# Performance work log

Measured on AMD Instinct MI355X. Metric: run time of the kernel, lower is better.

Reference implementation:

```python
import jax, jax.numpy as jnp
import numpy as np

N_CELLS = 2048
D_IN = 512
D_HID = 1024
D_OUT = 512
SYNC = 0.15
DEBATE = 0.15
N_FACTIONS = 8


def setup_inputs() -> dict:
    key = jax.random.key(0)
    ks = jax.random.split(key, 24)
    def w(k, shape, s=0.02):
        return jax.random.normal(k, shape, dtype=jnp.float32) * s
    ein = D_IN + D_HID          # complex-engine input dim (1536)
    gin = D_OUT + 1 + D_HID     # GRU gate input dim (1537)
    return {
        "x": jax.random.normal(ks[0], (1, D_IN), dtype=jnp.float32),
        "h_re": w(ks[1], (N_CELLS, D_HID), 0.1),
        "h_im": w(ks[2], (N_CELLS, D_HID), 0.1),
        "ea_wr": w(ks[3], (ein, D_OUT)), "ea_br": w(ks[4], (D_OUT,)),
        "ea_wi": w(ks[5], (ein, D_OUT)), "ea_bi": w(ks[6], (D_OUT,)),
        "eg_wr": w(ks[7], (ein, D_OUT)), "eg_br": w(ks[8], (D_OUT,)),
        "eg_wi": w(ks[9], (ein, D_OUT)), "eg_bi": w(ks[10], (D_OUT,)),
        "gz_w": w(ks[11], (gin, D_HID)), "gz_b": w(ks[12], (D_HID,)),
        "gr_w": w(ks[13], (gin, D_HID)), "gr_b": w(ks[14], (D_HID,)),
        "ghr_w": w(ks[15], (gin, D_HID)), "ghr_b": w(ks[16], (D_HID,)),
        "ghi_w": w(ks[17], (gin, D_HID)), "ghi_b": w(ks[18], (D_HID,)),
        "oh_w": w(ks[19], (2 * D_OUT, D_IN)), "oh_b": w(ks[20], (D_IN,)),
        "step": 7,
    }


def _clin(a, b, Wr, br, Wi, bi):
    # complex linear: (Wr + iWi)(a + ib) with torch's bias semantics
    return (a @ Wr + br) - (b @ Wi + bi), (b @ Wr + br) + (a @ Wi + bi)


def reference(x, h_re, h_im, ea_wr, ea_br, ea_wi, ea_bi, eg_wr, eg_br, eg_wi, eg_bi,
              gz_w, gz_b, gr_w, gr_b, ghr_w, ghr_b, ghi_w, ghi_b, oh_w, oh_b, step):
    # batch the 256-cell Python loop into single GEMMs over the cell axis
    xb = jnp.broadcast_to(x, (N_CELLS, D_IN))
    c_re = jnp.concatenate([xb, h_re], -1)                       # [N, D_IN+D_HID]
    c_im = jnp.concatenate([jnp.zeros_like(xb), h_im], -1)
    a_re, a_im = _clin(c_re, c_im, ea_wr, ea_br, ea_wi, ea_bi)
    g_re, g_im = _clin(c_re, c_im, eg_wr, eg_br, eg_wi, eg_bi)
    o_re, o_im = a_re - g_re, a_im - g_im                        # [N, D_OUT]
    tension = jnp.mean(o_re**2 + o_im**2, -1)                    # [N]

    # GRU memory update (detached input, matching output.detach())
    so_re = jax.lax.stop_gradient(o_re)
    so_im = jax.lax.stop_gradient(o_im)
    t_sg = jax.lax.stop_gradient(tension)
    mem_re = jnp.concatenate([so_re, t_sg[:, None]], -1)         # [N, D_OUT+1]
    mem_im = jnp.concatenate([so_im, jnp.zeros((N_CELLS, 1), o_im.dtype)], -1)
    x_mag = jnp.sqrt(mem_re**2 + mem_im**2)
    h_mag = jnp.sqrt(h_re**2 + h_im**2)
    cm = jnp.concatenate([x_mag, h_mag], -1)                     # [N, D_OUT+1+D_HID]
    z = jax.nn.sigmoid(cm @ gz_w + gz_b)
    r = jax.nn.sigmoid(cm @ gr_w + gr_b)
    comb_r = jnp.concatenate([mem_re, r * h_re], -1)
    comb_i = jnp.concatenate([mem_im, r * h_im], -1)
    cand_re = jnp.tanh(comb_r @ ghr_w + ghr_b)
    cand_im = jnp.tanh(comb_i @ ghi_w + ghi_b)
    nh_re = jax.lax.stop_gradient((1 - z) * h_re + z * cand_re)
    nh_im = jax.lax.stop_gradient((1 - z) * h_im + z * cand_im)

    # faction sync + debate (linear op, applied per component)
    fs = N_CELLS // N_FACTIONS
    def sync(h):
        hf = h.reshape(N_FACTIONS, fs, D_HID)
        hf = (1 - SYNC) * hf + SYNC * jnp.mean(hf, 1, keepdims=True)
        if step > 5:
            glob = jnp.mean(jnp.mean(hf, 1), 0)                  # [D_HID]
            dc = max(1, fs // 4)
            hf = hf.at[:, :dc].set((1 - DEBATE) * hf[:, :dc] + DEBATE * glob)
        return hf.reshape(N_CELLS, D_HID)
    nh_re, nh_im = sync(nh_re), sync(nh_im)

    # tension-softmax-weighted combination (weights are non-differentiable, .item() in torch)
    w_soft = jax.nn.softmax(t_sg)                                # [N]
    comb_re = (w_soft[:, None] * o_re).sum(0, keepdims=True)     # [1, D_OUT]
    comb_im = (w_soft[:, None] * o_im).sum(0, keepdims=True)
    out_real = jnp.concatenate([comb_re, comb_im], -1)           # [1, 2*D_OUT]
    pred = out_real @ oh_w + oh_b                                # [1, D_IN]
    return pred, jnp.mean(tension), nh_re, nh_im
```

## Files before the change

### kernel.cpp

```cpp
#include <hip/hip_runtime.h>
#include <math.h>

#define N_CELLS 2048
#define D_IN 512
#define D_HID 1024
#define D_OUT 512

typedef __attribute__((ext_vector_type(8))) short bf16x8;
typedef __attribute__((ext_vector_type(4))) float f32x4;
typedef __attribute__((ext_vector_type(4))) short short4v;

#define MFMA16(a, b, c) __builtin_amdgcn_mfma_f32_16x16x32_bf16(a, b, c, 0, 0, 0)

__device__ __forceinline__ short f2bf(float f) {
  union { float f; unsigned u; } v; v.f = f;
  unsigned r = (v.u + 0x7FFFu + ((v.u >> 16) & 1u)) >> 16;
  return (short)r;
}

__device__ __forceinline__ void gl_lds16(const void* g, void* l) {
  __builtin_amdgcn_global_load_lds(
      (const __attribute__((address_space(1))) void*)g,
      (__attribute__((address_space(3))) void*)l, 16, 0, 0);
}

__global__ __launch_bounds__(256) void k_transpose_all(
    const float* __restrict__ w0, const float* __restrict__ w1,
    const float* __restrict__ w2, const float* __restrict__ w3,
    short* __restrict__ t0, short* __restrict__ t1,
    short* __restrict__ t2, short* __restrict__ t3,
    const float* __restrict__ ea_wr, const float* __restrict__ eg_wr,
    const float* __restrict__ ea_wi, const float* __restrict__ eg_wi,
    short* __restrict__ wdrT, short* __restrict__ wdiT, short* __restrict__ wdnT) {
  const int k0 = blockIdx.x * 32, n0 = blockIdx.y * 32;
  const int c = threadIdx.x & 31, r4 = threadIdx.x >> 5;
  if (blockIdx.z < 4) {
    const float* w = (blockIdx.z == 0) ? w0 : (blockIdx.z == 1) ? w1
                   : (blockIdx.z == 2) ? w2 : w3;
    short* wT = (blockIdx.z == 0) ? t0 : (blockIdx.z == 1) ? t1
              : (blockIdx.z == 2) ? t2 : t3;
    __shared__ float t[32][33];
#pragma unroll
    for (int i = 0; i < 4; ++i) {
      int kl = r4 * 4 + i;
      int k = k0 + kl;
      int srcrow = (k < 512) ? k : k + 1;
      t[kl][c] = w[(size_t)srcrow * D_HID + n0 + c];
    }
    __syncthreads();
#pragma unroll
    for (int i = 0; i < 4; ++i) {
      int nl = r4 * 4 + i;
      wT[(size_t)(n0 + nl) * 1536 + k0 + c] = f2bf(t[c][nl]);
    }
  } else {
    if (blockIdx.x >= 32 || blockIdx.y >= 16) return;
    __shared__ float tr[32][33], ti[32][33];
#pragma unroll
    for (int i = 0; i < 4; ++i) {
      int kl = r4 * 4 + i;
      int src = (512 + k0 + kl) * D_OUT + n0 + c;
      tr[kl][c] = ea_wr[src] - eg_wr[src];
      ti[kl][c] = ea_wi[src] - eg_wi[src];
    }
    __syncthreads();
#pragma unroll
    for (int i = 0; i < 4; ++i) {
      int nl = r4 * 4 + i;
      int dst = (n0 + nl) * D_HID + k0 + c;
      float dr = tr[c][nl], di = ti[c][nl];
      wdrT[dst] = f2bf(dr);
      wdiT[dst] = f2bf(di);
      wdnT[dst] = f2bf(-di);
    }
  }
}

__global__ __launch_bounds__(256) void k_prep_h(
    const float* __restrict__ h_re, const float* __restrict__ h_im,
    short* __restrict__ hbre, short* __restrict__ hbim, short* __restrict__ gatesA,
    float* __restrict__ tens) {
  if (threadIdx.x == 0) tens[blockIdx.x] = 0.f;
  int idx4 = (blockIdx.x * 256 + threadIdx.x) * 4;
  int m = idx4 >> 10, n = idx4 & 1023;
  float4 hr = *(const float4*)&h_re[idx4];
  float4 hi = *(const float4*)&h_im[idx4];
  short4v br, bi, bm;
  br.x = f2bf(hr.x); br.y = f2bf(hr.y); br.z = f2bf(hr.z); br.w = f2bf(hr.w);
  bi.x = f2bf(hi.x); bi.y = f2bf(hi.y); bi.z = f2bf(hi.z); bi.w = f2bf(hi.w);
  bm.x = f2bf(sqrtf(hr.x * hr.x + hi.x * hi.x));
  bm.y = f2bf(sqrtf(hr.y * hr.y + hi.y * hi.y));
  bm.z = f2bf(sqrtf(hr.z * hr.z + hi.z * hi.z));
  bm.w = f2bf(sqrtf(hr.w * hr.w + hi.w * hi.w));
  *(short4v*)&hbre[idx4] = br;
  *(short4v*)&hbim[idx4] = bi;
  *(short4v*)&gatesA[(size_t)m * 1536 + 512 + n] = bm;
}

__global__ __launch_bounds__(256) void k_bias_part(
    const float* __restrict__ x,
    const float* __restrict__ ea_wr, const float* __restrict__ ea_wi,
    const float* __restrict__ eg_wr, const float* __restrict__ eg_wi,
    float* __restrict__ bpartr, float* __restrict__ bparti) {
  int n = blockIdx.x * 256 + threadIdx.x;
  int kc = blockIdx.y;
  float sr = 0.f, si = 0.f;
  for (int i = 0; i < 64; ++i) {
    int k = kc * 64 + i;
    float xv = x[k];
    int idx = k * D_OUT + n;
    sr += xv * (ea_wr[idx] - eg_wr[idx]);
    si += xv * (ea_wi[idx] - eg_wi[idx]);
  }
  bpartr[kc * D_OUT + n] = sr;
  bparti[kc * D_OUT + n] = si;
}

__global__ __launch_bounds__(256) void k_bias_red(
    const float* __restrict__ bpartr, const float* __restrict__ bparti,
    const float* __restrict__ ea_br, const float* __restrict__ ea_bi,
    const float* __restrict__ eg_br, const float* __restrict__ eg_bi,
    float* __restrict__ bias_re, float* __restrict__ bias_im) {
  int n = blockIdx.x * 256 + threadIdx.x;
  float sr = 0.f, si = 0.f;
#pragma unroll
  for (int kc = 0; kc < 8; ++kc) { sr += bpartr[kc * D_OUT + n]; si += bparti[kc * D_OUT + n]; }
  float brd = ea_br[n] - eg_br[n];
  float bid = ea_bi[n] - eg_bi[n];
  bias_re[n] = sr + brd - bid;
  bias_im[n] = si + brd + bid;
}

__global__ __launch_bounds__(256) void k_engine(
    const short* __restrict__ hbre, const short* __restrict__ hbim,
    const short* __restrict__ wdrT, const short* __restrict__ wdiT,
    const short* __restrict__ wdnT,
    const float* __restrict__ bias_re, const float* __restrict__ bias_im,
    float* __restrict__ ore, float* __restrict__ oim,
    short* __restrict__ gatesA, short* __restrict__ candAre, short* __restrict__ candAim,
    float* __restrict__ tens) {
  __shared__ short Ar[2 * 64 * 32], Ai[2 * 64 * 32];
  __shared__ short Brs[2 * 32 * 32], Bis[2 * 32 * 32], Bns[2 * 32 * 32];
  const int m0 = blockIdx.x * 64, n0 = blockIdx.y * 32;
  const int tid = threadIdx.x;
  const int wid = tid >> 6, lane = tid & 63;
  const int quad = lane >> 4, lcol = lane & 15;
  const int wm = wid * 16;
  f32x4 accre[2], accim[2];
#pragma unroll
  for (int nt = 0; nt < 2; ++nt) {
    accre[nt] = (f32x4){0.f, 0.f, 0.f, 0.f};
    accim[nt] = (f32x4){0.f, 0.f, 0.f, 0.f};
  }
  for (int k0 = 0; k0 < D_HID; k0 += 64) {
    if (k0) __syncthreads();
#pragma unroll
    for (int i = 0; i < 2; ++i) {
      int c = i * 256 + tid;
      int kh = c >> 8, row = (c >> 2) & 63, kq = c & 3;
      size_t g = (size_t)(m0 + row) * D_HID + k0 + kh * 32 + kq * 8;
      gl_lds16(hbre + g, &Ar[c * 8]);
      gl_lds16(hbim + g, &Ai[c * 8]);
    }
    {
      int c = tid;
      int kh = c >> 7, row = (c >> 2) & 31, kq = c & 3;
      size_t g = (size_t)(n0 + row) * D_HID + k0 + kh * 32 + kq * 8;
      gl_lds16(wdrT + g, &Brs[c * 8]);
      gl_lds16(wdiT + g, &Bis[c * 8]);
      gl_lds16(wdnT + g, &Bns[c * 8]);
    }
    __syncthreads();
#pragma unroll
    for (int kh = 0; kh < 2; ++kh) {
      bf16x8 ar, ai, br[2], bi[2], bn[2];
      int aoff = kh * 2048 + (wm + lcol) * 32 + quad * 8;
      ar = *(const bf16x8*)&Ar[aoff];
      ai = *(const bf16x8*)&Ai[aoff];
#pragma unroll
      for (int nt = 0; nt < 2; ++nt) {
        int boff = kh * 1024 + (nt * 16 + lcol) * 32 + quad * 8;
        br[nt] = *(const bf16x8*)&Brs[boff];
        bi[nt] = *(const bf16x8*)&Bis[boff];
        bn[nt] = *(const bf16x8*)&Bns[boff];
      }
#pragma unroll
      for (int nt = 0; nt < 2; ++nt) {
        accre[nt] = MFMA16(ar, br[nt], accre[nt]);
        accre[nt] = MFMA16(ai, bn[nt], accre[nt]);
        accim[nt] = MFMA16(ar, bi[nt], accim[nt]);
        accim[nt] = MFMA16(ai, br[nt], accim[nt]);
      }
    }
  }
#pragma unroll
  for (int r = 0; r < 4; ++r) {
    int m = m0 + wm + quad * 4 + r;
    float t = 0.f;
#pragma unroll
    for (int nt = 0; nt < 2; ++nt) {
      int n = n0 + nt * 16 + lcol;
      float cre = accre[nt][r] + bias_re[n];
      float cim = accim[nt][r] + bias_im[n];
      t += cre * cre + cim * cim;
      ore[(size_t)m * D_OUT + n] = cre;
      oim[(size_t)m * D_OUT + n] = cim;
      gatesA[(size_t)m * 1536 + n] = f2bf(sqrtf(cre * cre + cim * cim));
      candAre[(size_t)m * 1536 + n] = f2bf(cre);
      candAim[(size_t)m * 1536 + n] = f2bf(cim);
    }
#pragma unroll
    for (int off = 1; off < 16; off <<= 1) t += __shfl_xor(t, off);
    if (lcol == 0) atomicAdd(&tens[m], t * (1.f / 512.f));
  }
}

__global__ __launch_bounds__(256) void k_gates(
    const short* __restrict__ gatesA,
    const short* __restrict__ gzwT, const short* __restrict__ grwT,
    const float* __restrict__ gz_w, const float* __restrict__ gz_b,
    const float* __restrict__ gr_w, const float* __restrict__ gr_b,
    const float* __restrict__ tens,
    const float* __restrict__ h_re, const float* __restrict__ h_im,
    float* __restrict__ zbuf,
    short* __restrict__ candAre, short* __restrict__ candAim) {
  __shared__ short As[2 * 128 * 32];
  __shared__ short Bs[2 * 64 * 32];
  const int is_z = (blockIdx.z == 0);
  const short* Bt = is_z ? gzwT : grwT;
  const int m0 = blockIdx.x * 128, n0 = blockIdx.y * 64;
  const int tid = threadIdx.x;
  const int wid = tid >> 6, lane = tid & 63;
  const int quad = lane >> 4, lcol = lane & 15;
  const int wm = (wid >> 1) * 64, wn = (wid & 1) * 32;
  f32x4 acc[4][2];
#pragma unroll
  for (int mt = 0; mt < 4; ++mt)
#pragma unroll
    for (int nt = 0; nt < 2; ++nt) acc[mt][nt] = (f32x4){0.f, 0.f, 0.f, 0.f};
  for (int k0 = 0; k0 < 1536; k0 += 64) {
    if (k0) __syncthreads();
#pragma unroll
    for (int i = 0; i < 4; ++i) {
      int c = i * 256 + tid;
      int kh = c >> 9, row = (c >> 2) & 127, kq = c & 3;
      gl_lds16(gatesA + (size_t)(m0 + row) * 1536 + k0 + kh * 32 + kq * 8, &As[c * 8]);
    }
#pragma unroll
    for (int i = 0; i < 2; ++i) {
      int c = i * 256 + tid;
      int kh = c >> 8, row = (c >> 2) & 63, kq = c & 3;
      gl_lds16(Bt + (size_t)(n0 + row) * 1536 + k0 + kh * 32 + kq * 8, &Bs[c * 8]);
    }
    __syncthreads();
#pragma unroll
    for (int kh = 0; kh < 2; ++kh) {
      bf16x8 a[4], b[2];
#pragma unroll
      for (int mt = 0; mt < 4; ++mt)
        a[mt] = *(const bf16x8*)&As[kh * 4096 + (wm + mt * 16 + lcol) * 32 + quad * 8];
#pragma unroll
      for (int nt = 0; nt < 2; ++nt)
        b[nt] = *(const bf16x8*)&Bs[kh * 2048 + (wn + nt * 16 + lcol) * 32 + quad * 8];
#pragma unroll
      for (int mt = 0; mt < 4; ++mt)
#pragma unroll
        for (int nt = 0; nt < 2; ++nt)
          acc[mt][nt] = MFMA16(a[mt], b[nt], acc[mt][nt]);
    }
  }
#pragma unroll
  for (int mt = 0; mt < 4; ++mt)
#pragma unroll
    for (int nt = 0; nt < 2; ++nt)
#pragma unroll
      for (int r = 0; r < 4; ++r) {
        int m = m0 + wm + mt * 16 + quad * 4 + r;
        int n = n0 + wn + nt * 16 + lcol;
        float tv = tens[m];
        if (is_z) {
          float zp = acc[mt][nt][r] + gz_b[n] + tv * gz_w[(size_t)512 * D_HID + n];
          zbuf[(size_t)m * D_HID + n] = 1.f / (1.f + expf(-zp));
        } else {
          float rp = acc[mt][nt][r] + gr_b[n] + tv * gr_w[(size_t)512 * D_HID + n];
          float rr = 1.f / (1.f + expf(-rp));
          candAre[(size_t)m * 1536 + 512 + n] = f2bf(rr * h_re[(size_t)m * D_HID + n]);
          candAim[(size_t)m * 1536 + 512 + n] = f2bf(rr * h_im[(size_t)m * D_HID + n]);
        }
      }
}

__global__ __launch_bounds__(256) void k_cand(
    const short* __restrict__ candAre, const short* __restrict__ candAim,
    const short* __restrict__ ghrwT, const short* __restrict__ ghiwT,
    const float* __restrict__ ghr_b, const float* __restrict__ ghi_b,
    const float* __restrict__ ghr_w,
    const float* __restrict__ tens, const float* __restrict__ zbuf,
    const float* __restrict__ h_re, const float* __restrict__ h_im,
    float* __restrict__ nhre, float* __restrict__ nhim) {
  __shared__ short As[2 * 128 * 32];
  __shared__ short Bs[2 * 64 * 32];
  const int is_re = (blockIdx.z == 0);
  const short* A = is_re ? candAre : candAim;
  const short* Bt = is_re ? ghrwT : ghiwT;
  const float* bias = is_re ? ghr_b : ghi_b;
  const float* h = is_re ? h_re : h_im;
  float* outp = is_re ? nhre : nhim;
  const int m0 = blockIdx.x * 128, n0 = blockIdx.y * 64;
  const int tid = threadIdx.x;
  const int wid = tid >> 6, lane = tid & 63;
  const int quad = lane >> 4, lcol = lane & 15;
  const int wm = (wid >> 1) * 64, wn = (wid & 1) * 32;
  f32x4 acc[4][2];
#pragma unroll
  for (int mt = 0; mt < 4; ++mt)
#pragma unroll
    for (int nt = 0; nt < 2; ++nt) acc[mt][nt] = (f32x4){0.f, 0.f, 0.f, 0.f};
  for (int k0 = 0; k0 < 1536; k0 += 64) {
    if (k0) __syncthreads();
#pragma unroll
    for (int i = 0; i < 4; ++i) {
      int c = i * 256 + tid;
      int kh = c >> 9, row = (c >> 2) & 127, kq = c & 3;
      gl_lds16(A + (size_t)(m0 + row) * 1536 + k0 + kh * 32 + kq * 8, &As[c * 8]);
    }
#pragma unroll
    for (int i = 0; i < 2; ++i) {
      int c = i * 256 + tid;
      int kh = c >> 8, row = (c >> 2) & 63, kq = c & 3;
      gl_lds16(Bt + (size_t)(n0 + row) * 1536 + k0 + kh * 32 + kq * 8, &Bs[c * 8]);
    }
    __syncthreads();
#pragma unroll
    for (int kh = 0; kh < 2; ++kh) {
      bf16x8 a[4], b[2];
#pragma unroll
      for (int mt = 0; mt < 4; ++mt)
        a[mt] = *(const bf16x8*)&As[kh * 4096 + (wm + mt * 16 + lcol) * 32 + quad * 8];
#pragma unroll
      for (int nt = 0; nt < 2; ++nt)
        b[nt] = *(const bf16x8*)&Bs[kh * 2048 + (wn + nt * 16 + lcol) * 32 + quad * 8];
#pragma unroll
      for (int mt = 0; mt < 4; ++mt)
#pragma unroll
        for (int nt = 0; nt < 2; ++nt)
          acc[mt][nt] = MFMA16(a[mt], b[nt], acc[mt][nt]);
    }
  }
#pragma unroll
  for (int mt = 0; mt < 4; ++mt)
#pragma unroll
    for (int nt = 0; nt < 2; ++nt)
#pragma unroll
      for (int r = 0; r < 4; ++r) {
        int m = m0 + wm + mt * 16 + quad * 4 + r;
        int n = n0 + wn + nt * 16 + lcol;
        float pre = acc[mt][nt][r] + bias[n];
        if (is_re) pre += tens[m] * ghr_w[(size_t)512 * D_HID + n];
        float cand = tanhf(pre);
        float z = zbuf[(size_t)m * D_HID + n];
        float hv = h[(size_t)m * D_HID + n];
        outp[(size_t)m * D_HID + n] = (1.f - z) * hv + z * cand;
      }
}

__global__ __launch_bounds__(256) void k_fsum_part(
    const float* __restrict__ nhre, const float* __restrict__ nhim,
    float* __restrict__ fpart) {
  int f = blockIdx.x >> 3, rc = blockIdx.x & 7, comp = blockIdx.y;
  const float* src = comp ? nhim : nhre;
  int row0 = f * 256 + rc * 32;
#pragma unroll
  for (int nc = 0; nc < 4; ++nc) {
    int n = nc * 256 + threadIdx.x;
    float s = 0.f;
    const float* base = src + (size_t)row0 * D_HID + n;
    for (int j = 0; j < 32; ++j) s += base[(size_t)j * D_HID];
    fpart[((size_t)comp * 64 + blockIdx.x) * D_HID + n] = s;
  }
}

__global__ __launch_bounds__(256) void k_fsum_red(
    const float* __restrict__ fpart,
    float* __restrict__ fsre, float* __restrict__ fsim,
    float* __restrict__ gre, float* __restrict__ gim) {
  int n = blockIdx.x * 256 + threadIdx.x;
  int comp = blockIdx.y;
  float* fs = comp ? fsim : fsre;
  float* g = comp ? gim : gre;
  float gsum = 0.f;
#pragma unroll
  for (int f = 0; f < 8; ++f) {
    float sf = 0.f;
#pragma unroll
    for (int rc = 0; rc < 8; ++rc)
      sf += fpart[((size_t)comp * 64 + f * 8 + rc) * D_HID + n];
    fs[f * D_HID + n] = sf;
    gsum += sf;
  }
  g[n] = gsum * (1.f / 2048.f);
}

__global__ __launch_bounds__(256) void k_sync(
    float* __restrict__ nhre, float* __restrict__ nhim,
    const float* __restrict__ fsre, const float* __restrict__ fsim,
    const float* __restrict__ gre, const float* __restrict__ gim,
    const int* __restrict__ step) {
  int idx = blockIdx.x * 256 + threadIdx.x;
  int m = idx >> 10, n = idx & 1023;
  int f = m >> 8;
  float vr = nhre[idx], vi = nhim[idx];
  vr = 0.85f * vr + 0.15f * (fsre[f * D_HID + n] * (1.f / 256.f));
  vi = 0.85f * vi + 0.15f * (fsim[f * D_HID + n] * (1.f / 256.f));
  if (step[0] > 5 && (m & 255) < 64) {
    vr = 0.85f * vr + 0.15f * gre[n];
    vi = 0.85f * vi + 0.15f * gim[n];
  }
  nhre[idx] = vr;
  nhim[idx] = vi;
}

__global__ __launch_bounds__(1024) void k_stats(
    const float* __restrict__ tens, float* __restrict__ wsoft,
    float* __restrict__ meanT_out) {
  __shared__ float red[16];
  __shared__ float s_max, s_sum;
  int tid = threadIdx.x;
  int wid = tid >> 6, lane = tid & 63;
  float a = tens[tid], b = tens[tid + 1024];
  float mx = fmaxf(a, b);
  for (int off = 32; off; off >>= 1) mx = fmaxf(mx, __shfl_down(mx, off));
  if (lane == 0) red[wid] = mx;
  __syncthreads();
  if (tid == 0) {
    float m2 = red[0];
    for (int i = 1; i < 16; ++i) m2 = fmaxf(m2, red[i]);
    s_max = m2;
  }
  __syncthreads();
  float mxv = s_max;
  float ea = expf(a - mxv), eb = expf(b - mxv);
  float se = ea + eb;
  for (int off = 32; off; off >>= 1) se += __shfl_down(se, off);
  __syncthreads();
  if (lane == 0) red[wid] = se;
  __syncthreads();
  if (tid == 0) {
    float s2 = 0.f;
    for (int i = 0; i < 16; ++i) s2 += red[i];
    s_sum = s2;
  }
  __syncthreads();
  float inv = 1.f / s_sum;
  wsoft[tid] = ea * inv;
  wsoft[tid + 1024] = eb * inv;
  float st = a + b;
  for (int off = 32; off; off >>= 1) st += __shfl_down(st, off);
  __syncthreads();
  if (lane == 0) red[wid] = st;
  __syncthreads();
  if (tid == 0) {
    float s2 = 0.f;
    for (int i = 0; i < 16; ++i) s2 += red[i];
    meanT_out[0] = s2 * (1.f / 2048.f);
  }
}

__global__ __launch_bounds__(256) void k_comb_part(
    const float* __restrict__ ore, const float* __restrict__ oim,
    const float* __restrict__ wsoft, float* __restrict__ cpart) {
  int j = blockIdx.x * 256 + threadIdx.x;
  int mc = blockIdx.y;
  const float* src = (j < 512) ? ore : oim;
  int col = j & 511;
  float s = 0.f;
  for (int i = 0; i < 128; ++i) {
    int m = mc * 128 + i;
    s += wsoft[m] * src[(size_t)m * D_OUT + col];
  }
  cpart[(size_t)mc * 1024 + j] = s;
}

__global__ __launch_bounds__(256) void k_pred_part(
    const float* __restrict__ cpart, const float* __restrict__ oh_w,
    float* __restrict__ ppart) {
  __shared__ float combs[128];
  int tid = threadIdx.x;
  int jc = blockIdx.y;
  if (tid < 128) {
    float s = 0.f;
#pragma unroll
    for (int mc = 0; mc < 16; ++mc) s += cpart[(size_t)mc * 1024 + jc * 128 + tid];
    combs[tid] = s;
  }
  __syncthreads();
  int n = blockIdx.x * 256 + tid;
  float s = 0.f;
  for (int i = 0; i < 128; ++i)
    s += combs[i] * oh_w[(size_t)(jc * 128 + i) * D_IN + n];
  ppart[(size_t)jc * D_IN + n] = s;
}

__global__ __launch_bounds__(256) void k_pred_red(
    const float* __restrict__ ppart, const float* __restrict__ oh_b,
    float* __restrict__ pred) {
  int n = blockIdx.x * 256 + threadIdx.x;
  float s = oh_b[n];
#pragma unroll
  for (int jc = 0; jc < 8; ++jc) s += ppart[(size_t)jc * D_IN + n];
  pred[n] = s;
}

extern "C" void kernel_launch(void* const* d_in, const int* in_sizes, int n_in,
                              void* d_out, int out_size, void* d_ws, size_t ws_size,
                              hipStream_t stream) {
  const float* x     = (const float*)d_in[0];
  const float* h_re  = (const float*)d_in[1];
  const float* h_im  = (const float*)d_in[2];
  const float* ea_wr = (const float*)d_in[3];
  const float* ea_br = (const float*)d_in[4];
  const float* ea_wi = (const float*)d_in[5];
  const float* ea_bi = (const float*)d_in[6];
  const float* eg_wr = (const float*)d_in[7];
  const float* eg_br = (const float*)d_in[8];
  const float* eg_wi = (const float*)d_in[9];
  const float* eg_bi = (const float*)d_in[10];
  const float* gz_w  = (const float*)d_in[11];
  const float* gz_b  = (const float*)d_in[12];
  const float* gr_w  = (const float*)d_in[13];
  const float* gr_b  = (const float*)d_in[14];
  const float* ghr_w = (const float*)d_in[15];
  const float* ghr_b = (const float*)d_in[16];
  const float* ghi_w = (const float*)d_in[17];
  const float* ghi_b = (const float*)d_in[18];
  const float* oh_w  = (const float*)d_in[19];
  const float* oh_b  = (const float*)d_in[20];
  const int*   step  = (const int*)d_in[21];

  float* out = (float*)d_out;
  float* pred_out  = out;
  float* meanT_out = out + 512;
  float* nhre_out  = out + 513;
  float* nhim_out  = out + 513 + N_CELLS * D_HID;

  char* p = (char*)d_ws;
  auto carve = [&](size_t bytes) { char* r = p; p += (bytes + 255) & ~(size_t)255; return r; };
  short* wdrT   = (short*)carve(512 * 1024 * 2);
  short* wdiT   = (short*)carve(512 * 1024 * 2);
  short* wdnT   = (short*)carve(512 * 1024 * 2);
  short* gzwT   = (short*)carve(1024 * 1536 * 2);
  short* grwT   = (short*)carve(1024 * 1536 * 2);
  short* ghrwT  = (short*)carve(1024 * 1536 * 2);
  short* ghiwT  = (short*)carve(1024 * 1536 * 2);
  short* hbre   = (short*)carve(2048 * 1024 * 2);
  short* hbim   = (short*)carve(2048 * 1024 * 2);
  short* gatesA = (short*)carve((size_t)2048 * 1536 * 2);
  short* candAre= (short*)carve((size_t)2048 * 1536 * 2);
  short* candAim= (short*)carve((size_t)2048 * 1536 * 2);
  float* ore    = (float*)carve(2048 * 512 * 4);
  float* oim    = (float*)carve(2048 * 512 * 4);
  float* zbuf   = (float*)carve((size_t)2048 * 1024 * 4);
  float* bias_re= (float*)carve(512 * 4);
  float* bias_im= (float*)carve(512 * 4);
  float* bpartr = (float*)carve(8 * 512 * 4);
  float* bparti = (float*)carve(8 * 512 * 4);
  float* tens   = (float*)carve(2048 * 4);
  float* fpart  = (float*)carve(2 * 64 * 1024 * 4);
  float* fsre   = (float*)carve(8 * 1024 * 4);
  float* fsim   = (float*)carve(8 * 1024 * 4);
  float* gre    = (float*)carve(1024 * 4);
  float* gim    = (float*)carve(1024 * 4);
  float* wsoft  = (float*)carve(2048 * 4);
  float* cpart  = (float*)carve(16 * 1024 * 4);
  float* ppart  = (float*)carve(8 * 512 * 4);

  hipLaunchKernelGGL(k_transpose_all, dim3(48, 32, 5), dim3(256), 0, stream,
                     gz_w, gr_w, ghr_w, ghi_w, gzwT, grwT, ghrwT, ghiwT,
                     ea_wr, eg_wr, ea_wi, eg_wi, wdrT, wdiT, wdnT);
  hipLaunchKernelGGL(k_prep_h, dim3(2048), dim3(256), 0, stream,
                     h_re, h_im, hbre, hbim, gatesA, tens);
  hipLaunchKernelGGL(k_bias_part, dim3(2, 8), dim3(256), 0, stream,
                     x, ea_wr, ea_wi, eg_wr, eg_wi, bpartr, bparti);
  hipLaunchKernelGGL(k_bias_red, dim3(2), dim3(256), 0, stream,
                     bpartr, bparti, ea_br, ea_bi, eg_br, eg_bi, bias_re, bias_im);
  hipLaunchKernelGGL(k_engine, dim3(32, 16), dim3(256), 0, stream,
                     hbre, hbim, wdrT, wdiT, wdnT, bias_re, bias_im,
                     ore, oim, gatesA, candAre, candAim, tens);
  hipLaunchKernelGGL(k_gates, dim3(16, 16, 2), dim3(256), 0, stream,
                     gatesA, gzwT, grwT, gz_w, gz_b, gr_w, gr_b, tens,
                     h_re, h_im, zbuf, candAre, candAim);
  hipLaunchKernelGGL(k_cand, dim3(16, 16, 2), dim3(256), 0, stream,
                     candAre, candAim, ghrwT, ghiwT, ghr_b, ghi_b, ghr_w,
                     tens, zbuf, h_re, h_im, nhre_out, nhim_out);
  hipLaunchKernelGGL(k_fsum_part, dim3(64, 2), dim3(256), 0, stream,
                     nhre_out, nhim_out, fpart);
  hipLaunchKernelGGL(k_fsum_red, dim3(4, 2), dim3(256), 0, stream,
                     fpart, fsre, fsim, gre, gim);
  hipLaunchKernelGGL(k_sync, dim3((N_CELLS * D_HID) / 256), dim3(256), 0, stream,
                     nhre_out, nhim_out, fsre, fsim, gre, gim, step);
  hipLaunchKernelGGL(k_stats, dim3(1), dim3(1024), 0, stream, tens, wsoft, meanT_out);
  hipLaunchKernelGGL(k_comb_part, dim3(4, 16), dim3(256), 0, stream,
                     ore, oim, wsoft, cpart);
  hipLaunchKernelGGL(k_pred_part, dim3(2, 8), dim3(256), 0, stream, cpart, oh_w, ppart);
  hipLaunchKernelGGL(k_pred_red, dim3(2), dim3(256), 0, stream, ppart, oh_b, pred_out);
}
```

Baseline: 290.9 us.

## Replace LDS-staged GEMM tiles with direct global-to-register MFMA operand loads

The three GEMM kernels (engine, gates, cand) drop shared-memory staging via global_load_lds and the __syncthreads barriers. Instead each wave loads its bf16x8 MFMA fragments straight from global memory into registers, relying on the L1/L2 caches for reuse. The engine kernel's per-wave tile also grows to 32 rows, which halves its grid. This removes barrier and LDS traffic, but operands shared across waves are now fetched redundantly from cache, and the 16-byte-per-lane row-strided loads may coalesce poorly.

```diff
diff --git a/kernel.cpp b/kernel.cpp
--- a/kernel.cpp
+++ b/kernel.cpp
@@ -16,12 +16,6 @@
   union { float f; unsigned u; } v; v.f = f;
   unsigned r = (v.u + 0x7FFFu + ((v.u >> 16) & 1u)) >> 16;
   return (short)r;
-}
-
-__device__ __forceinline__ void gl_lds16(const void* g, void* l) {
-  __builtin_amdgcn_global_load_lds(
-      (const __attribute__((address_space(1))) void*)g,
-      (__attribute__((address_space(3))) void*)l, 16, 0, 0);
 }
 
 __global__ __launch_bounds__(256) void k_transpose_all(
@@ -139,80 +133,73 @@
     float* __restrict__ ore, float* __restrict__ oim,
     short* __restrict__ gatesA, short* __restrict__ candAre, short* __restrict__ candAim,
     float* __restrict__ tens) {
-  __shared__ short Ar[2 * 64 * 32], Ai[2 * 64 * 32];
-  __shared__ short Brs[2 * 32 * 32], Bis[2 * 32 * 32], Bns[2 * 32 * 32];
-  const int m0 = blockIdx.x * 64, n0 = blockIdx.y * 32;
-  const int tid = threadIdx.x;
-  const int wid = tid >> 6, lane = tid & 63;
+  const int tid = threadIdx.x, wid = tid >> 6, lane = tid & 63;
   const int quad = lane >> 4, lcol = lane & 15;
-  const int wm = wid * 16;
-  f32x4 accre[2], accim[2];
-#pragma unroll
-  for (int nt = 0; nt < 2; ++nt) {
-    accre[nt] = (f32x4){0.f, 0.f, 0.f, 0.f};
-    accim[nt] = (f32x4){0.f, 0.f, 0.f, 0.f};
-  }
-  for (int k0 = 0; k0 < D_HID; k0 += 64) {
-    if (k0) __syncthreads();
-#pragma unroll
-    for (int i = 0; i < 2; ++i) {
-      int c = i * 256 + tid;
-      int kh = c >> 8, row = (c >> 2) & 63, kq = c & 3;
-      size_t g = (size_t)(m0 + row) * D_HID + k0 + kh * 32 + kq * 8;
-      gl_lds16(hbre + g, &Ar[c * 8]);
-      gl_lds16(hbim + g, &Ai[c * 8]);
+  const int m0 = blockIdx.x * 128 + wid * 32;
+  const int n0 = blockIdx.y * 32;
+  const short* pAr0 = hbre + (size_t)(m0 + lcol) * D_HID + quad * 8;
+  const short* pAr1 = hbre + (size_t)(m0 + 16 + lcol) * D_HID + quad * 8;
+  const short* pAi0 = hbim + (size_t)(m0 + lcol) * D_HID + quad * 8;
+  const short* pAi1 = hbim + (size_t)(m0 + 16 + lcol) * D_HID + quad * 8;
+  const short* pBr0 = wdrT + (size_t)(n0 + lcol) * D_HID + quad * 8;
+  const short* pBr1 = wdrT + (size_t)(n0 + 16 + lcol) * D_HID + quad * 8;
+  const short* pBi0 = wdiT + (size_t)(n0 + lcol) * D_HID + quad * 8;
+  const short* pBi1 = wdiT + (size_t)(n0 + 16 + lcol) * D_HID + quad * 8;
+  const short* pBn0 = wdnT + (size_t)(n0 + lcol) * D_HID + quad * 8;
+  const short* pBn1 = wdnT + (size_t)(n0 + 16 + lcol) * D_HID + quad * 8;
+  f32x4 accre[2][2], accim[2][2];
+#pragma unroll
+  for (int mt = 0; mt < 2; ++mt)
+#pragma unroll
+    for (int nt = 0; nt < 2; ++nt) {
+      accre[mt][nt] = (f32x4){0.f, 0.f, 0.f, 0.f};
+      accim[mt][nt] = (f32x4){0.f, 0.f, 0.f, 0.f};
     }
-    {
-      int c = tid;
-      int kh = c >> 7, row = (c >> 2) & 31, kq = c & 3;
-      size_t g = (size_t)(n0 + row) * D_HID + k0 + kh * 32 + kq * 8;
-      gl_lds16(wdrT + g, &Brs[c * 8]);
-      gl_lds16(wdiT + g, &Bis[c * 8]);
-      gl_lds16(wdnT + g, &Bns[c * 8]);
+#pragma unroll 4
+  for (int kk = 0; kk < 32; ++kk) {
+    bf16x8 ar[2], ai[2], br[2], bi[2], bn[2];
+    ar[0] = *(const bf16x8*)pAr0; pAr0 += 32;
+    ar[1] = *(const bf16x8*)pAr1; pAr1 += 32;
+    ai[0] = *(const bf16x8*)pAi0; pAi0 += 32;
+    ai[1] = *(const bf16x8*)pAi1; pAi1 += 32;
+    br[0] = *(const bf16x8*)pBr0; pBr0 += 32;
+    br[1] = *(const bf16x8*)pBr1; pBr1 += 32;
+    bi[0] = *(const bf16x8*)pBi0; pBi0 += 32;
+    bi[1] = *(const bf16x8*)pBi1; pBi1 += 32;
+    bn[0] = *(const bf16x8*)pBn0; pBn0 += 32;
+    bn[1] = *(const bf16x8*)pBn1; pBn1 += 32;
+#pragma unroll
+    for (int mt = 0; mt < 2; ++mt)
+#pragma unroll
+      for (int nt = 0; nt < 2; ++nt) {
+        accre[mt][nt] = MFMA16(ar[mt], br[nt], accre[mt][nt]);
+        accre[mt][nt] = MFMA16(ai[mt], bn[nt], accre[mt][nt]);
+        accim[mt][nt] = MFMA16(ar[mt], bi[nt], accim[mt][nt]);
+        accim[mt][nt] = MFMA16(ai[mt], br[nt], accim[mt][nt]);
+      }
+  }
+#pragma unroll
+  for (int mt = 0; mt < 2; ++mt)
+#pragma unroll
+    for (int r = 0; r < 4; ++r) {
+      int m = m0 + mt * 16 + quad * 4 + r;
+      float t = 0.f;
+#pragma unroll
+      for (int nt = 0; nt < 2; ++nt) {
+        int n = n0 + nt * 16 + lcol;
+        float cre = accre[mt][nt][r] + bias_re[n];
+        float cim = accim[mt][nt][r] + bias_im[n];
+        t += cre * cre + cim * cim;
+        ore[(size_t)m * D_OUT + n] = cre;
+        oim[(size_t)m * D_OUT + n] = cim;
+        gatesA[(size_t)m * 1536 + n] = f2bf(sqrtf(cre * cre + cim * cim));
+        candAre[(size_t)m * 1536 + n] = f2bf(cre);
+        candAim[(size_t)m * 1536 + n] = f2bf(cim);
+      }
+#pragma unroll
+      for (int off = 1; off < 16; off <<= 1) t += __shfl_xor(t, off);
+      if (lcol == 0) atomicAdd(&tens[m], t * (1.f / 512.f));
     }
-    __syncthreads();
-#pragma unroll
-    for (int kh = 0; kh < 2; ++kh) {
-      bf16x8 ar, ai, br[2], bi[2], bn[2];
-      int aoff = kh * 2048 + (wm + lcol) * 32 + quad * 8;
-      ar = *(const bf16x8*)&Ar[aoff];
-      ai = *(const bf16x8*)&Ai[aoff];
-#pragma unroll
-      for (int nt = 0; nt < 2; ++nt) {
-        int boff = kh * 1024 + (nt * 16 + lcol) * 32 + quad * 8;
-        br[nt] = *(const bf16x8*)&Brs[boff];
-        bi[nt] = *(const bf16x8*)&Bis[boff];
-        bn[nt] = *(const bf16x8*)&Bns[boff];
-      }
-#pragma unroll
-      for (int nt = 0; nt < 2; ++nt) {
-        accre[nt] = MFMA16(ar, br[nt], accre[nt]);
-        accre[nt] = MFMA16(ai, bn[nt], accre[nt]);
-        accim[nt] = MFMA16(ar, bi[nt], accim[nt]);
-        accim[nt] = MFMA16(ai, br[nt], accim[nt]);
-      }
-    }
-  }
-#pragma unroll
-  for (int r = 0; r < 4; ++r) {
-    int m = m0 + wm + quad * 4 + r;
-    float t = 0.f;
-#pragma unroll
-    for (int nt = 0; nt < 2; ++nt) {
-      int n = n0 + nt * 16 + lcol;
-      float cre = accre[nt][r] + bias_re[n];
-      float cim = accim[nt][r] + bias_im[n];
-      t += cre * cre + cim * cim;
-      ore[(size_t)m * D_OUT + n] = cre;
-      oim[(size_t)m * D_OUT + n] = cim;
-      gatesA[(size_t)m * 1536 + n] = f2bf(sqrtf(cre * cre + cim * cim));
-      candAre[(size_t)m * 1536 + n] = f2bf(cre);
-      candAim[(size_t)m * 1536 + n] = f2bf(cim);
-    }
-#pragma unroll
-    for (int off = 1; off < 16; off <<= 1) t += __shfl_xor(t, off);
-    if (lcol == 0) atomicAdd(&tens[m], t * (1.f / 512.f));
-  }
 }
 
 __global__ __launch_bounds__(256) void k_gates(
@@ -224,59 +211,48 @@
     const float* __restrict__ h_re, const float* __restrict__ h_im,
     float* __restrict__ zbuf,
     short* __restrict__ candAre, short* __restrict__ candAim) {
-  __shared__ short As[2 * 128 * 32];
-  __shared__ short Bs[2 * 64 * 32];
   const int is_z = (blockIdx.z == 0);
   const short* Bt = is_z ? gzwT : grwT;
-  const int m0 = blockIdx.x * 128, n0 = blockIdx.y * 64;
-  const int tid = threadIdx.x;
-  const int wid = tid >> 6, lane = tid & 63;
+  const int tid = threadIdx.x, wid = tid >> 6, lane = tid & 63;
   const int quad = lane >> 4, lcol = lane & 15;
-  const int wm = (wid >> 1) * 64, wn = (wid & 1) * 32;
-  f32x4 acc[4][2];
-#pragma unroll
-  for (int mt = 0; mt < 4; ++mt)
-#pragma unroll
-    for (int nt = 0; nt < 2; ++nt) acc[mt][nt] = (f32x4){0.f, 0.f, 0.f, 0.f};
-  for (int k0 = 0; k0 < 1536; k0 += 64) {
-    if (k0) __syncthreads();
-#pragma unroll
-    for (int i = 0; i < 4; ++i) {
-      int c = i * 256 + tid;
-      int kh = c >> 9, row = (c >> 2) & 127, kq = c & 3;
-      gl_lds16(gatesA + (size_t)(m0 + row) * 1536 + k0 + kh * 32 + kq * 8, &As[c * 8]);
-    }
-#pragma unroll
-    for (int i = 0; i < 2; ++i) {
-      int c = i * 256 + tid;
-      int kh = c >> 8, row = (c >> 2) & 63, kq = c & 3;
-      gl_lds16(Bt + (size_t)(n0 + row) * 1536 + k0 + kh * 32 + kq * 8, &Bs[c * 8]);
-    }
-    __syncthreads();
-#pragma unroll
-    for (int kh = 0; kh < 2; ++kh) {
-      bf16x8 a[4], b[2];
-#pragma unroll
-      for (int mt = 0; mt < 4; ++mt)
-        a[mt] = *(const bf16x8*)&As[kh * 4096 + (wm + mt * 16 + lcol) * 32 + quad * 8];
-#pragma unroll
-      for (int nt = 0; nt < 2; ++nt)
-        b[nt] = *(const bf16x8*)&Bs[kh * 2048 + (wn + nt * 16 + lcol) * 32 + quad * 8];
-#pragma unroll
-      for (int mt = 0; mt < 4; ++mt)
-#pragma unroll
-        for (int nt = 0; nt < 2; ++nt)
-          acc[mt][nt] = MFMA16(a[mt], b[nt], acc[mt][nt]);
-    }
-  }
-#pragma unroll
-  for (int mt = 0; mt < 4; ++mt)
-#pragma unroll
-    for (int nt = 0; nt < 2; ++nt)
+  const int m0 = blockIdx.x * 128 + wid * 32;
+  const int n0 = blockIdx.y * 64;
+  const short* pA0 = gatesA + (size_t)(m0 + lcol) * 1536 + quad * 8;
+  const short* pA1 = gatesA + (size_t)(m0 + 16 + lcol) * 1536 + quad * 8;
+  const short* pB0 = Bt + (size_t)(n0 + lcol) * 1536 + quad * 8;
+  const short* pB1 = Bt + (size_t)(n0 + 16 + lcol) * 1536 + quad * 8;
+  const short* pB2 = Bt + (size_t)(n0 + 32 + lcol) * 1536 + quad * 8;
+  const short* pB3 = Bt + (size_t)(n0 + 48 + lcol) * 1536 + quad * 8;
+  f32x4 acc[2][4];
+#pragma unroll
+  for (int mt = 0; mt < 2; ++mt)
+#pragma unroll
+    for (int nt = 0; nt < 4; ++nt) acc[mt][nt] = (f32x4){0.f, 0.f, 0.f, 0.f};
+#pragma unroll 4
+  for (int kk = 0; kk < 48; ++kk) {
+    bf16x8 a0 = *(const bf16x8*)pA0; pA0 += 32;
+    bf16x8 a1 = *(const bf16x8*)pA1; pA1 += 32;
+    bf16x8 b0 = *(const bf16x8*)pB0; pB0 += 32;
+    bf16x8 b1 = *(const bf16x8*)pB1; pB1 += 32;
+    bf16x8 b2 = *(const bf16x8*)pB2; pB2 += 32;
+    bf16x8 b3 = *(const bf16x8*)pB3; pB3 += 32;
+    acc[0][0] = MFMA16(a0, b0, acc[0][0]);
+    acc[0][1] = MFMA16(a0, b1, acc[0][1]);
+    acc[0][2] = MFMA16(a0, b2, acc[0][2]);
+    acc[0][3] = MFMA16(a0, b3, acc[0][3]);
+    acc[1][0] = MFMA16(a1, b0, acc[1][0]);
+    acc[1][1] = MFMA16(a1, b1, acc[1][1]);
+    acc[1][2] = MFMA16(a1, b2, acc[1][2]);
+    acc[1][3] = MFMA16(a1, b3, acc[1][3]);
+  }
+#pragma unroll
+  for (int mt = 0; mt < 2; ++mt)
+#pragma unroll
+    for (int nt = 0; nt < 4; ++nt)
 #pragma unroll
       for (int r = 0; r < 4; ++r) {
-        int m = m0 + wm + mt * 16 + quad * 4 + r;
-        int n = n0 + wn + nt * 16 + lcol;
+        int m = m0 + mt * 16 + quad * 4 + r;
+        int n = n0 + nt * 16 + lcol;
         float tv = tens[m];
         if (is_z) {
           float zp = acc[mt][nt][r] + gz_b[n] + tv * gz_w[(size_t)512 * D_HID + n];
@@ -298,63 +274,52 @@
     const float* __restrict__ tens, const float* __restrict__ zbuf,
     const float* __restrict__ h_re, const float* __restrict__ h_im,
     float* __restrict__ nhre, float* __restrict__ nhim) {
-  __shared__ short As[2 * 128 * 32];
-  __shared__ short Bs[2 * 64 * 32];
   const int is_re = (blockIdx.z == 0);
   const short* A = is_re ? candAre : candAim;
   const short* Bt = is_re ? ghrwT : ghiwT;
   const float* bias = is_re ? ghr_b : ghi_b;
   const float* h = is_re ? h_re : h_im;
   float* outp = is_re ? nhre : nhim;
-  const int m0 = blockIdx.x * 128, n0 = blockIdx.y * 64;
-  const int tid = threadIdx.x;
-  const int wid = tid >> 6, lane = tid & 63;
+  const int tid = threadIdx.x, wid = tid >> 6, lane = tid & 63;
   const int quad = lane >> 4, lcol = lane & 15;
-  const int wm = (wid >> 1) * 64, wn = (wid & 1) * 32;
-  f32x4 acc[4][2];
-#pragma unroll
-  for (int mt = 0; mt < 4; ++mt)
-#pragma unroll
-    for (int nt = 0; nt < 2; ++nt) acc[mt][nt] = (f32x4){0.f, 0.f, 0.f, 0.f};
-  for (int k0 = 0; k0 < 1536; k0 += 64) {
-    if (k0) __syncthreads();
-#pragma unroll
-    for (int i = 0; i < 4; ++i) {
-      int c = i * 256 + tid;
-      int kh = c >> 9, row = (c >> 2) & 127, kq = c & 3;
-      gl_lds16(A + (size_t)(m0 + row) * 1536 + k0 + kh * 32 + kq * 8, &As[c * 8]);
-    }
-#pragma unroll
-    for (int i = 0; i < 2; ++i) {
-      int c = i * 256 + tid;
-      int kh = c >> 8, row = (c >> 2) & 63, kq = c & 3;
-      gl_lds16(Bt + (size_t)(n0 + row) * 1536 + k0 + kh * 32 + kq * 8, &Bs[c * 8]);
-    }
-    __syncthreads();
-#pragma unroll
-    for (int kh = 0; kh < 2; ++kh) {
-      bf16x8 a[4], b[2];
-#pragma unroll
-      for (int mt = 0; mt < 4; ++mt)
-        a[mt] = *(const bf16x8*)&As[kh * 4096 + (wm + mt * 16 + lcol) * 32 + quad * 8];
-#pragma unroll
-      for (int nt = 0; nt < 2; ++nt)
-        b[nt] = *(const bf16x8*)&Bs[kh * 2048 + (wn + nt * 16 + lcol) * 32 + quad * 8];
-#pragma unroll
-      for (int mt = 0; mt < 4; ++mt)
-#pragma unroll
-        for (int nt = 0; nt < 2; ++nt)
-          acc[mt][nt] = MFMA16(a[mt], b[nt], acc[mt][nt]);
-    }
-  }
-#pragma unroll
-  for (int mt = 0; mt < 4; ++mt)
-#pragma unroll
-    for (int nt = 0; nt < 2; ++nt)
+  const int m0 = blockIdx.x * 128 + wid * 32;
+  const int n0 = blockIdx.y * 64;
+  const short* pA0 = A + (size_t)(m0 + lcol) * 1536 + quad * 8;
+  const short* pA1 = A + (size_t)(m0 + 16 + lcol) * 1536 + quad * 8;
+  const short* pB0 = Bt + (size_t)(n0 + lcol) * 1536 + quad * 8;
+  const short* pB1 = Bt + (size_t)(n0 + 16 + lcol) * 1536 + quad * 8;
+  const short* pB2 = Bt + (size_t)(n0 + 32 + lcol) * 1536 + quad * 8;
+  const short* pB3 = Bt + (size_t)(n0 + 48 + lcol) * 1536 + quad * 8;
+  f32x4 acc[2][4];
+#pragma unroll
+  for (int mt = 0; mt < 2; ++mt)
+#pragma unroll
+    for (int nt = 0; nt < 4; ++nt) acc[mt][nt] = (f32x4){0.f, 0.f, 0.f, 0.f};
+#pragma unroll 4
+  for (int kk = 0; kk < 48; ++kk) {
+    bf16x8 a0 = *(const bf16x8*)pA0; pA0 += 32;
+    bf16x8 a1 = *(const bf16x8*)pA1; pA1 += 32;
+    bf16x8 b0 = *(const bf16x8*)pB0; pB0 += 32;
+    bf16x8 b1 = *(const bf16x8*)pB1; pB1 += 32;
+    bf16x8 b2 = *(const bf16x8*)pB2; pB2 += 32;
+    bf16x8 b3 = *(const bf16x8*)pB3; pB3 += 32;
+    acc[0][0] = MFMA16(a0, b0, acc[0][0]);
+    acc[0][1] = MFMA16(a0, b1, acc[0][1]);
+    acc[0][2] = MFMA16(a0, b2, acc[0][2]);
+    acc[0][3] = MFMA16(a0, b3, acc[0][3]);
+    acc[1][0] = MFMA16(a1, b0, acc[1][0]);
+    acc[1][1] = MFMA16(a1, b1, acc[1][1]);
+    acc[1][2] = MFMA16(a1, b2, acc[1][2]);
+    acc[1][3] = MFMA16(a1, b3, acc[1][3]);
+  }
+#pragma unroll
+  for (int mt = 0; mt < 2; ++mt)
+#pragma unroll
+    for (int nt = 0; nt < 4; ++nt)
 #pragma unroll
       for (int r = 0; r < 4; ++r) {
-        int m = m0 + wm + mt * 16 + quad * 4 + r;
-        int n = n0 + wn + nt * 16 + lcol;
+        int m = m0 + mt * 16 + quad * 4 + r;
+        int n = n0 + nt * 16 + lcol;
         float pre = acc[mt][nt][r] + bias[n];
         if (is_re) pre += tens[m] * ghr_w[(size_t)512 * D_HID + n];
         float cand = tanhf(pre);
@@ -583,7 +548,7 @@
                      x, ea_wr, ea_wi, eg_wr, eg_wi, bpartr, bparti);
   hipLaunchKernelGGL(k_bias_red, dim3(2), dim3(256), 0, stream,
                      bpartr, bparti, ea_br, ea_bi, eg_br, eg_bi, bias_re, bias_im);
-  hipLaunchKernelGGL(k_engine, dim3(32, 16), dim3(256), 0, stream,
+  hipLaunchKernelGGL(k_engine, dim3(16, 16), dim3(256), 0, stream,
                      hbre, hbim, wdrT, wdiT, wdnT, bias_re, bias_im,
                      ore, oim, gatesA, candAre, candAim, tens);
   hipLaunchKernelGGL(k_gates, dim3(16, 16, 2), dim3(256), 0, stream,
```

Result: slower. 394.8 us (+35.7%).
